# Kernel tuning notes

Measured on AMD Instinct MI355X. Metric: run time of the kernel, lower is better.

Reference implementation:

```python
import jax, jax.numpy as jnp
import numpy as np

B = 8192
D_IN, D1, D2, D3, D_OUT = 784, 256, 1024, 256, 10
N_STEPS = 20
LR_INFER = 0.1
GAMMA = 0.1


def setup_inputs() -> dict:
    key = jax.random.key(0)
    ks = jax.random.split(key, 17)
    inp = {
        "x": jax.random.normal(ks[0], (B, D_IN), dtype=jnp.float32),
        # state inits (original does randn*0.1 inside forward)
        "x1_0": jax.random.normal(ks[1], (B, D1), dtype=jnp.float32) * 0.1,
        "x2_0": jax.random.normal(ks[2], (B, D2), dtype=jnp.float32) * 0.1,
        "x3_0": jax.random.normal(ks[3], (B, D3), dtype=jnp.float32) * 0.1,
        "x4_0": jax.random.normal(ks[4], (B, D_OUT), dtype=jnp.float32) * 0.1,
        # parameters (randn*0.1 per __init__)
        "W1": jax.random.normal(ks[5], (D_IN, D1), dtype=jnp.float32) * 0.1,
        "W2": jax.random.normal(ks[6], (D1, D2), dtype=jnp.float32) * 0.1,
        "W3": jax.random.normal(ks[7], (D2, D3), dtype=jnp.float32) * 0.1,
        "W4": jax.random.normal(ks[8], (D3, D_OUT), dtype=jnp.float32) * 0.1,
        "b1": jnp.zeros((D1,), dtype=jnp.float32),
        "b2": jnp.zeros((D2,), dtype=jnp.float32),
        "b3": jnp.zeros((D3,), dtype=jnp.float32),
        "b4": jnp.zeros((D_OUT,), dtype=jnp.float32),
        "L1": jax.random.normal(ks[9], (D1, D1), dtype=jnp.float32) * 0.1,
        "L2": jax.random.normal(ks[10], (D2, D2), dtype=jnp.float32) * 0.1,
        "L3": jax.random.normal(ks[11], (D3, D3), dtype=jnp.float32) * 0.1,
    }
    return inp


def reference(x, x1_0, x2_0, x3_0, x4_0, W1, W2, W3, W4, b1, b2, b3, b4, L1, L2, L3):
    sig = jax.nn.sigmoid
    # x1_pred depends only on the (constant) input x; compute once.
    x1_pred = sig(x @ W1 + b1)  # [B, D1]

    def step(carry, _):
        x1, x2, x3 = carry
        x3_pred = sig(x2 @ W3 + b3)        # [B, D3]
        x2_pred = sig(x1 @ W2 + b2)        # [B, D2]
        x4_pred = x3 @ W4 + b4             # [B, D_OUT]
        eps4 = x4_pred - x4_0
        eps3 = x3_pred - x3
        eps2 = x2_pred - x2
        eps1 = x1_pred - x1
        x3_grad = -eps3 + eps4 @ W4.T - GAMMA * (x3 @ L3)
        x2_grad = -eps2 + eps3 @ W3.T - GAMMA * (x2 @ L2)
        x1_grad = -eps1 + eps2 @ W2.T - GAMMA * (x1 @ L1)
        return (x1 - LR_INFER * x1_grad,
                x2 - LR_INFER * x2_grad,
                x3 - LR_INFER * x3_grad), None

    (x1, x2, x3), _ = jax.lax.scan(step, (x1_0, x2_0, x3_0), None, length=N_STEPS)
    return x3 @ W4 + b4  # [B, D_OUT]
```

## Files before the change

kernel.cpp:

```cpp
#include <hip/hip_runtime.h>
#include <hip/hip_bf16.h>
#include <cstdint>
#include <cstring>


#define LRC 0.1f

typedef unsigned short u16;
typedef unsigned int u32;
typedef __attribute__((ext_vector_type(4))) float f32x4;
typedef __attribute__((ext_vector_type(8))) __bf16 bf16x8;

__device__ __forceinline__ u16 f2b(float v) {
  __hip_bfloat16 h = __float2bfloat16(v);
  union { __hip_bfloat16 h; u16 u; } c; c.h = h; return c.u;
}
__device__ __forceinline__ float b2f(u16 u) {
  union { u16 u; __hip_bfloat16 h; } c; c.u = u; return __bfloat162float(c.h);
}
__device__ __forceinline__ float sigf(float x) { return 1.0f / (1.0f + expf(-x)); }

__device__ __forceinline__ void gll16(const void* g, void* l) {
  __builtin_amdgcn_global_load_lds((const __attribute__((address_space(1))) u32*)g,
                                   (__attribute__((address_space(3))) u32*)l,
                                   16, 0, 0);
}

struct GemmDesc {
  const u16* A; const u16* Bt;
  const u16* A2; const u16* Bt2;
  const float* bias; const float* master; const float* pred; const float* aux;
  const u16* eprev;
  float* outF; u16* outB;
  int lda, ldb, lda2, ldb2, K, K2, N, tnl, nblocks, epi;
};
struct Descs { GemmDesc d[6]; int nd; };

__global__ __launch_bounds__(256) void k_gemm_multi(Descs P) {
  int bid = blockIdx.x;
  int base = 0, di = 0;
  while (di + 1 < P.nd && bid >= base + P.d[di].nblocks) { base += P.d[di].nblocks; ++di; }
  const GemmDesc& d = P.d[di];
  int t = bid - base;
  int tid = threadIdx.x;

  __shared__ u16 ldsA[8192];
  __shared__ u16 ldsB[8192];

  int w = tid >> 6, l = tid & 63;
  int wm = w & 1, wn = w >> 1;
  int lrow = l & 15, kgrp = l >> 4;

  int tnl = d.tnl;
  int j = t >> 3;
  int tm = (t & 7) * (d.nblocks >> (3 + tnl)) + (j >> tnl);
  int tnn = j & ((1 << tnl) - 1);
  int m0 = tm * 128, n0 = tnn * 128;

  f32x4 zero = {0.f, 0.f, 0.f, 0.f};
  f32x4 acc[4][4];
  #pragma unroll
  for (int a = 0; a < 4; ++a)
    #pragma unroll
    for (int b = 0; b < 4; ++b) acc[a][b] = zero;

  int srow = l >> 2;
  int scol = (l & 3) * 8;

  auto run = [&](const u16* A, int lda, const u16* Bt, int ldb, int K) {
    for (int k0 = 0; k0 < K;) {
      int nsub = (K - k0 >= 64) ? 2 : 1;
      for (int i = 0; i < 2 * nsub; ++i) {
        int c = i * 4 + w;
        int ks = c >> 3, rb = c & 7;
        int row = rb * 16 + srow;
        int col = k0 + ks * 32 + scol;
        gll16(A  + (size_t)(m0 + row) * lda + col, &ldsA[c * 512]);
        gll16(Bt + (size_t)(n0 + row) * ldb + col, &ldsB[c * 512]);
      }
      __syncthreads();
      for (int ks = 0; ks < nsub; ++ks) {
        bf16x8 af[4], bfr[4];
        #pragma unroll
        for (int mi = 0; mi < 4; ++mi)
          af[mi] = *(const bf16x8*)&ldsA[ks * 4096 + (wm * 64 + mi * 16 + lrow) * 32 + kgrp * 8];
        #pragma unroll
        for (int ni = 0; ni < 4; ++ni)
          bfr[ni] = *(const bf16x8*)&ldsB[ks * 4096 + (wn * 64 + ni * 16 + lrow) * 32 + kgrp * 8];
        #pragma unroll
        for (int mi = 0; mi < 4; ++mi)
          #pragma unroll
          for (int ni = 0; ni < 4; ++ni)
            acc[mi][ni] = __builtin_amdgcn_mfma_f32_16x16x32_bf16(af[mi], bfr[ni], acc[mi][ni], 0, 0, 0);
      }
      __syncthreads();
      k0 += nsub * 32;
    }
  };

  run(d.A, d.lda, d.Bt, d.ldb, d.K);
  if (d.K2 > 0) run(d.A2, d.lda2, d.Bt2, d.ldb2, d.K2);

  int epi = d.epi;
  #pragma unroll
  for (int mi = 0; mi < 4; ++mi) {
    #pragma unroll
    for (int ni = 0; ni < 4; ++ni) {
      #pragma unroll
      for (int j2 = 0; j2 < 4; ++j2) {
        int row = m0 + wm * 64 + mi * 16 + kgrp * 4 + j2;
        int col = n0 + wn * 64 + ni * 16 + lrow;
        size_t idx = (size_t)row * d.N + col;
        float a = acc[mi][ni][j2];
        if (epi == 1) {
          float s = sigf(a + d.bias[col]);
          d.outB[idx] = f2b(s - b2f(d.eprev[idx]));
        } else if (epi == 2) {
          d.outF[idx] = sigf(a + d.bias[col]);
        } else if (epi == 3) {
          float v = d.outF[idx];
          float nv = v + LRC * (d.pred[idx] - v) - LRC * a;
          d.outF[idx] = nv; d.outB[idx] = f2b(nv);
        } else if (epi == 4) {
          float v = d.outF[idx];
          float nv = v + LRC * b2f(d.eprev[idx]) - LRC * a;
          d.outF[idx] = nv; d.outB[idx] = f2b(nv);
        } else {
          float v = d.outF[idx];
          float nv = v + LRC * b2f(d.eprev[idx]) - LRC * (a + d.pred[idx]);
          d.outF[idx] = nv; d.outB[idx] = f2b(nv);
        }
      }
    }
  }
}

__global__ void k_state_init(const float* __restrict__ src, float* __restrict__ dstF,
                             u16* __restrict__ dstB, int n) {
  int i = blockIdx.x * 256 + threadIdx.x;
  if (i < n) { float v = src[i]; dstF[i] = v; dstB[i] = f2b(v); }
}
__global__ void k_transpose_scale(const float* __restrict__ src, u16* __restrict__ dst,
                                  int R, int C, float scale) {
  int i = blockIdx.x * 256 + threadIdx.x;
  if (i < R * C) { int r = i / C, c = i - r * C; dst[c * R + r] = f2b(scale * src[i]); }
}
__global__ void k_conv_bf(const float* __restrict__ src, u16* __restrict__ dst, int n) {
  int i = blockIdx.x * 256 + threadIdx.x;
  if (i < n) dst[i] = f2b(src[i]);
}
__global__ void k_m4g(const float* __restrict__ W4, const float* __restrict__ L3,
                      u16* __restrict__ dst) {
  int i = blockIdx.x * 256 + threadIdx.x;
  if (i < 256 * 256) {
    int n = i >> 8, k = i & 255;
    float s = 0.f;
    #pragma unroll
    for (int jj = 0; jj < 10; ++jj) s = fmaf(W4[n * 10 + jj], W4[k * 10 + jj], s);
    dst[i] = f2b(s - 0.1f * L3[k * 256 + n]);
  }
}
__global__ void k_c4(const float* __restrict__ W4, const float* __restrict__ b4,
                     const float* __restrict__ x40, float* __restrict__ dst) {
  int i = blockIdx.x * 256 + threadIdx.x;
  if (i < 8192 * 256) {
    int m = i >> 8, n = i & 255;
    float s = 0.f;
    #pragma unroll
    for (int jj = 0; jj < 10; ++jj) s = fmaf(b4[jj] - x40[m * 10 + jj], W4[n * 10 + jj], s);
    dst[i] = s;
  }
}
__global__ void k_xsplit(const float* __restrict__ x, u16* __restrict__ dst) {
  int i = blockIdx.x * 256 + threadIdx.x;
  if (i < 8192 * 1600) {
    int m = i / 1600, c = i - m * 1600;
    u16 o = 0;
    if (c < 784) o = f2b(x[m * 784 + c]);
    else if (c >= 800 && c < 1584) {
      float v = x[m * 784 + (c - 800)];
      float h = b2f(f2b(v));
      o = f2b(v - h);
    }
    dst[i] = o;
  }
}
__global__ void k_w1c(const float* __restrict__ W1, u16* __restrict__ dst) {
  int i = blockIdx.x * 256 + threadIdx.x;
  if (i < 256 * 1600) {
    int n = i / 1600, c = i - n * 1600;
    u16 o = 0;
    if (c < 784) o = f2b(W1[c * 256 + n]);
    else if (c >= 800 && c < 1584) o = f2b(W1[(c - 800) * 256 + n]);
    dst[i] = o;
  }
}
__global__ void k_final(const float* __restrict__ X3, const float* __restrict__ W4,
                        const float* __restrict__ b4, float* __restrict__ out) {
  int i = blockIdx.x * 256 + threadIdx.x;
  if (i < 8192 * 10) {
    int m = i / 10, n = i - m * 10;
    const float* xr = X3 + (size_t)m * 256;
    float acc = 0.f;
    #pragma unroll 4
    for (int k = 0; k < 256; ++k) acc = fmaf(xr[k], W4[k * 10 + n], acc);
    out[i] = acc + b4[n];
  }
}

extern "C" void kernel_launch(void* const* d_in, const int* in_sizes, int n_in,
                              void* d_out, int out_size, void* d_ws, size_t ws_size,
                              hipStream_t stream) {
  const float* x    = (const float*)d_in[0];
  const float* x1_0 = (const float*)d_in[1];
  const float* x2_0 = (const float*)d_in[2];
  const float* x3_0 = (const float*)d_in[3];
  const float* x4_0 = (const float*)d_in[4];
  const float* W1 = (const float*)d_in[5];
  const float* W2 = (const float*)d_in[6];
  const float* W3 = (const float*)d_in[7];
  const float* W4 = (const float*)d_in[8];
  const float* b1 = (const float*)d_in[9];
  const float* b2 = (const float*)d_in[10];
  const float* b3 = (const float*)d_in[11];
  const float* b4 = (const float*)d_in[12];
  const float* L1 = (const float*)d_in[13];
  const float* L2 = (const float*)d_in[14];
  const float* L3 = (const float*)d_in[15];

  if (ws_size < 143687680u) return;
  char* ws = (char*)d_ws;
  float* X1f   = (float*)(ws + 0);
  float* X2f   = (float*)(ws + 8388608);
  float* X3f   = (float*)(ws + 41943040);
  u16*   X1b[2]= { (u16*)(ws + 50331648), (u16*)(ws + 54525952) };
  u16*   X2b[2]= { (u16*)(ws + 58720256), (u16*)(ws + 75497472) };
  u16*   X3b[2]= { (u16*)(ws + 92274688), (u16*)(ws + 96468992) };
  float* P1    = (float*)(ws + 100663296);
  u16*   E2    = (u16*)(ws + 109051904);
  u16*   E3    = (u16*)(ws + 125829120);
  float* C4    = (float*)(ws + 130023424);
  u16*   XS    = (u16*)(ws + 109051904);
  u16*   W2t   = (u16*)(ws + 138412032);
  u16*   W3t   = (u16*)(ws + 138936320);
  u16*   L1t   = (u16*)(ws + 139460608);
  u16*   L2t   = (u16*)(ws + 139591680);
  u16*   M4G   = (u16*)(ws + 141688832);
  u16*   W2b   = (u16*)(ws + 141819904);
  u16*   W3b   = (u16*)(ws + 142344192);
  u16*   W1c   = (u16*)(ws + 142868480);

  dim3 blk(256);
  auto G = [](int n) { return dim3((unsigned)((n + 255) / 256)); };

  k_state_init<<<G(8192*256),  blk, 0, stream>>>(x1_0, X1f, X1b[0], 8192*256);
  k_state_init<<<G(8192*1024), blk, 0, stream>>>(x2_0, X2f, X2b[0], 8192*1024);
  k_state_init<<<G(8192*256),  blk, 0, stream>>>(x3_0, X3f, X3b[0], 8192*256);
  k_transpose_scale<<<G(256*1024),  blk, 0, stream>>>(W2, W2t, 256, 1024, 1.0f);
  k_transpose_scale<<<G(1024*256),  blk, 0, stream>>>(W3, W3t, 1024, 256, 1.0f);
  k_transpose_scale<<<G(256*256),   blk, 0, stream>>>(L1, L1t, 256, 256, -0.1f);
  k_transpose_scale<<<G(1024*1024), blk, 0, stream>>>(L2, L2t, 1024, 1024, -0.1f);
  k_conv_bf<<<G(256*1024), blk, 0, stream>>>(W2, W2b, 256*1024);
  k_conv_bf<<<G(1024*256), blk, 0, stream>>>(W3, W3b, 1024*256);
  k_m4g<<<G(256*256), blk, 0, stream>>>(W4, L3, M4G);
  k_xsplit<<<G(8192*1600), blk, 0, stream>>>(x, XS);
  k_w1c<<<G(256*1600), blk, 0, stream>>>(W1, W1c);

  auto mkg = [](const u16* A, const u16* Bt, int lda, int ldb, int K, int N,
                int tnl, int nb, int epi) {
    GemmDesc g; memset(&g, 0, sizeof(g));
    g.A = A; g.Bt = Bt; g.lda = lda; g.ldb = ldb; g.K = K; g.N = N;
    g.tnl = tnl; g.nblocks = nb; g.epi = epi;
    return g;
  };

  {
    Descs pp; memset(&pp, 0, sizeof(pp)); pp.nd = 1;
    pp.d[0] = mkg(XS, W1c, 1600, 1600, 1600, 256, 1, 128, 2);
    pp.d[0].bias = b1; pp.d[0].outF = P1;
    k_gemm_multi<<<dim3(128), blk, 0, stream>>>(pp);
  }
  k_c4<<<G(8192*256), blk, 0, stream>>>(W4, b4, x4_0, C4);

  for (int s = 0; s < 20; ++s) {
    int p = s & 1, q = p ^ 1;

    Descs ph1; memset(&ph1, 0, sizeof(ph1)); ph1.nd = 2;
    ph1.d[0] = mkg(X2b[p], W3t, 1024, 1024, 1024, 256, 1, 128, 1);
    ph1.d[0].bias = b3; ph1.d[0].eprev = X3b[p]; ph1.d[0].outB = E3;
    ph1.d[1] = mkg(X1b[p], W2t, 256, 256, 256, 1024, 3, 512, 1);
    ph1.d[1].bias = b2; ph1.d[1].eprev = X2b[p]; ph1.d[1].outB = E2;
    k_gemm_multi<<<dim3(640), blk, 0, stream>>>(ph1);

    Descs ph2; memset(&ph2, 0, sizeof(ph2)); ph2.nd = 3;
    ph2.d[0] = mkg(E3, W3b, 256, 256, 256, 1024, 3, 512, 4);
    ph2.d[0].A2 = X2b[p]; ph2.d[0].Bt2 = L2t; ph2.d[0].lda2 = 1024;
    ph2.d[0].ldb2 = 1024; ph2.d[0].K2 = 1024;
    ph2.d[0].eprev = E2; ph2.d[0].outF = X2f; ph2.d[0].outB = X2b[q];
    ph2.d[1] = mkg(E2, W2b, 1024, 1024, 1024, 256, 1, 128, 3);
    ph2.d[1].A2 = X1b[p]; ph2.d[1].Bt2 = L1t; ph2.d[1].lda2 = 256;
    ph2.d[1].ldb2 = 256; ph2.d[1].K2 = 256;
    ph2.d[1].pred = P1; ph2.d[1].outF = X1f; ph2.d[1].outB = X1b[q];
    ph2.d[2] = mkg(X3b[p], M4G, 256, 256, 256, 256, 1, 128, 6);
    ph2.d[2].eprev = E3; ph2.d[2].pred = C4;
    ph2.d[2].outF = X3f; ph2.d[2].outB = X3b[q];
    k_gemm_multi<<<dim3(768), blk, 0, stream>>>(ph2);
  }

  k_final<<<G(81920), blk, 0, stream>>>(X3f, W4, b4, (float*)d_out);
}
```

Before: 2.333 ms.

## Load A fragments directly to registers with double-buffered prefetch in multi-GEMM kernel

```diff
diff --git a/kernel.cpp b/kernel.cpp
--- a/kernel.cpp
+++ b/kernel.cpp
@@ -44,7 +44,6 @@
   int t = bid - base;
   int tid = threadIdx.x;
 
-  __shared__ u16 ldsA[8192];
   __shared__ u16 ldsB[8192];
 
   int w = tid >> 6, l = tid & 63;
@@ -67,39 +66,66 @@
   int srow = l >> 2;
   int scol = (l & 3) * 8;
 
-  auto run = [&](const u16* A, int lda, const u16* Bt, int ldb, int K) {
-    for (int k0 = 0; k0 < K;) {
-      int nsub = (K - k0 >= 64) ? 2 : 1;
-      for (int i = 0; i < 2 * nsub; ++i) {
-        int c = i * 4 + w;
-        int ks = c >> 3, rb = c & 7;
-        int row = rb * 16 + srow;
-        int col = k0 + ks * 32 + scol;
-        gll16(A  + (size_t)(m0 + row) * lda + col, &ldsA[c * 512]);
-        gll16(Bt + (size_t)(n0 + row) * ldb + col, &ldsB[c * 512]);
-      }
-      __syncthreads();
-      for (int ks = 0; ks < nsub; ++ks) {
-        bf16x8 af[4], bfr[4];
-        #pragma unroll
-        for (int mi = 0; mi < 4; ++mi)
-          af[mi] = *(const bf16x8*)&ldsA[ks * 4096 + (wm * 64 + mi * 16 + lrow) * 32 + kgrp * 8];
+  int T1 = d.K >> 6;
+  int T  = T1 + (d.K2 >> 6);
+
+  auto loadA = [&](int vt, bf16x8* af) {
+    const u16* A; int lda, k0;
+    if (vt < T1) { A = d.A;  lda = d.lda;  k0 = vt << 6; }
+    else         { A = d.A2; lda = d.lda2; k0 = (vt - T1) << 6; }
+    #pragma unroll
+    for (int ks = 0; ks < 2; ++ks)
+      #pragma unroll
+      for (int mi = 0; mi < 4; ++mi)
+        af[ks * 4 + mi] = *(const bf16x8*)(A +
+            (size_t)(m0 + wm * 64 + mi * 16 + lrow) * lda + (k0 + ks * 32 + kgrp * 8));
+  };
+
+  auto stageB = [&](int vt) {
+    const u16* Bt; int ldb, k0;
+    if (vt < T1) { Bt = d.Bt;  ldb = d.ldb;  k0 = vt << 6; }
+    else         { Bt = d.Bt2; ldb = d.ldb2; k0 = (vt - T1) << 6; }
+    #pragma unroll
+    for (int i = 0; i < 4; ++i) {
+      int c = i * 4 + w;
+      int ks = c >> 3, rb = c & 7;
+      gll16(Bt + (size_t)(n0 + rb * 16 + srow) * ldb + (k0 + ks * 32 + scol),
+            &ldsB[c * 512]);
+    }
+  };
+
+  auto compute = [&](const bf16x8* af) {
+    #pragma unroll
+    for (int ks = 0; ks < 2; ++ks) {
+      bf16x8 bfr[4];
+      #pragma unroll
+      for (int ni = 0; ni < 4; ++ni)
+        bfr[ni] = *(const bf16x8*)&ldsB[ks * 4096 + (wn * 64 + ni * 16 + lrow) * 32 + kgrp * 8];
+      #pragma unroll
+      for (int mi = 0; mi < 4; ++mi)
         #pragma unroll
         for (int ni = 0; ni < 4; ++ni)
-          bfr[ni] = *(const bf16x8*)&ldsB[ks * 4096 + (wn * 64 + ni * 16 + lrow) * 32 + kgrp * 8];
-        #pragma unroll
-        for (int mi = 0; mi < 4; ++mi)
-          #pragma unroll
-          for (int ni = 0; ni < 4; ++ni)
-            acc[mi][ni] = __builtin_amdgcn_mfma_f32_16x16x32_bf16(af[mi], bfr[ni], acc[mi][ni], 0, 0, 0);
-      }
-      __syncthreads();
-      k0 += nsub * 32;
+          acc[mi][ni] = __builtin_amdgcn_mfma_f32_16x16x32_bf16(af[ks * 4 + mi], bfr[ni], acc[mi][ni], 0, 0, 0);
     }
   };
 
-  run(d.A, d.lda, d.Bt, d.ldb, d.K);
-  if (d.K2 > 0) run(d.A2, d.lda2, d.Bt2, d.ldb2, d.K2);
+  bf16x8 a0[8], a1[8];
+  loadA(0, a0);
+  stageB(0);
+  __syncthreads();
+  for (int vt = 0; vt < T; vt += 2) {
+    if (vt + 1 < T) loadA(vt + 1, a1);
+    compute(a0);
+    __syncthreads();
+    if (vt + 1 < T) stageB(vt + 1);
+    __syncthreads();
+    if (vt + 1 >= T) break;
+    if (vt + 2 < T) loadA(vt + 2, a0);
+    compute(a1);
+    __syncthreads();
+    if (vt + 2 < T) stageB(vt + 2);
+    __syncthreads();
+  }
 
   int epi = d.epi;
   #pragma unroll
```

Result: slower. 4.954 ms (+112.4%).

## Fuse all iteration GEMM phases into one persistent cooperative kernel with grid sync

Applied to the files above, without the earlier changes.

```diff
diff --git a/kernel.cpp b/kernel.cpp
--- a/kernel.cpp
+++ b/kernel.cpp
@@ -1,10 +1,13 @@
 #include <hip/hip_runtime.h>
 #include <hip/hip_bf16.h>
+#include <hip/hip_cooperative_groups.h>
 #include <cstdint>
 #include <cstring>
 
 
 #define LRC 0.1f
+
+namespace cg = cooperative_groups;
 
 typedef unsigned short u16;
 typedef unsigned int u32;
@@ -35,17 +38,16 @@
   int lda, ldb, lda2, ldb2, K, K2, N, tnl, nblocks, epi;
 };
 struct Descs { GemmDesc d[6]; int nd; };
-
-__global__ __launch_bounds__(256) void k_gemm_multi(Descs P) {
-  int bid = blockIdx.x;
+struct AllDesc { GemmDesc ph1[2][2]; GemmDesc ph2[2][3]; };
+
+__device__ void do_gemm(const GemmDesc* __restrict__ dd, int nd, int bid, int tid) {
   int base = 0, di = 0;
-  while (di + 1 < P.nd && bid >= base + P.d[di].nblocks) { base += P.d[di].nblocks; ++di; }
-  const GemmDesc& d = P.d[di];
+  while (di + 1 < nd && bid >= base + dd[di].nblocks) { base += dd[di].nblocks; ++di; }
+  const GemmDesc& d = dd[di];
   int t = bid - base;
-  int tid = threadIdx.x;
-
-  __shared__ u16 ldsA[8192];
-  __shared__ u16 ldsB[8192];
+
+  static __shared__ u16 ldsA[8192];
+  static __shared__ u16 ldsB[8192];
 
   int w = tid >> 6, l = tid & 63;
   int wm = w & 1, wn = w >> 1;
@@ -135,6 +137,24 @@
   }
 }
 
+__global__ __launch_bounds__(256) void k_gemm_multi(Descs P) {
+  do_gemm(P.d, P.nd, blockIdx.x, threadIdx.x);
+}
+
+__global__ __launch_bounds__(256, 3) void k_steps(AllDesc P) {
+  cg::grid_group g = cg::this_grid();
+  int tid = threadIdx.x;
+  for (int s = 0; s < 20; ++s) {
+    int p = s & 1;
+    for (int job = blockIdx.x; job < 640; job += gridDim.x)
+      do_gemm(P.ph1[p], 2, job, tid);
+    g.sync();
+    for (int job = blockIdx.x; job < 768; job += gridDim.x)
+      do_gemm(P.ph2[p], 3, job, tid);
+    g.sync();
+  }
+}
+
 __global__ void k_state_init(const float* __restrict__ src, float* __restrict__ dstF,
                              u16* __restrict__ dstB, int n) {
   int i = blockIdx.x * 256 + threadIdx.x;
@@ -282,29 +302,40 @@
   }
   k_c4<<<G(8192*256), blk, 0, stream>>>(W4, b4, x4_0, C4);
 
-  for (int s = 0; s < 20; ++s) {
-    int p = s & 1, q = p ^ 1;
-
-    Descs ph1; memset(&ph1, 0, sizeof(ph1)); ph1.nd = 2;
-    ph1.d[0] = mkg(X2b[p], W3t, 1024, 1024, 1024, 256, 1, 128, 1);
-    ph1.d[0].bias = b3; ph1.d[0].eprev = X3b[p]; ph1.d[0].outB = E3;
-    ph1.d[1] = mkg(X1b[p], W2t, 256, 256, 256, 1024, 3, 512, 1);
-    ph1.d[1].bias = b2; ph1.d[1].eprev = X2b[p]; ph1.d[1].outB = E2;
-    k_gemm_multi<<<dim3(640), blk, 0, stream>>>(ph1);
-
-    Descs ph2; memset(&ph2, 0, sizeof(ph2)); ph2.nd = 3;
-    ph2.d[0] = mkg(E3, W3b, 256, 256, 256, 1024, 3, 512, 4);
-    ph2.d[0].A2 = X2b[p]; ph2.d[0].Bt2 = L2t; ph2.d[0].lda2 = 1024;
-    ph2.d[0].ldb2 = 1024; ph2.d[0].K2 = 1024;
-    ph2.d[0].eprev = E2; ph2.d[0].outF = X2f; ph2.d[0].outB = X2b[q];
-    ph2.d[1] = mkg(E2, W2b, 1024, 1024, 1024, 256, 1, 128, 3);
-    ph2.d[1].A2 = X1b[p]; ph2.d[1].Bt2 = L1t; ph2.d[1].lda2 = 256;
-    ph2.d[1].ldb2 = 256; ph2.d[1].K2 = 256;
-    ph2.d[1].pred = P1; ph2.d[1].outF = X1f; ph2.d[1].outB = X1b[q];
-    ph2.d[2] = mkg(X3b[p], M4G, 256, 256, 256, 256, 1, 128, 6);
-    ph2.d[2].eprev = E3; ph2.d[2].pred = C4;
-    ph2.d[2].outF = X3f; ph2.d[2].outB = X3b[q];
-    k_gemm_multi<<<dim3(768), blk, 0, stream>>>(ph2);
+  AllDesc AD; memset(&AD, 0, sizeof(AD));
+  for (int p = 0; p < 2; ++p) {
+    int q = p ^ 1;
+    AD.ph1[p][0] = mkg(X2b[p], W3t, 1024, 1024, 1024, 256, 1, 128, 1);
+    AD.ph1[p][0].bias = b3; AD.ph1[p][0].eprev = X3b[p]; AD.ph1[p][0].outB = E3;
+    AD.ph1[p][1] = mkg(X1b[p], W2t, 256, 256, 256, 1024, 3, 512, 1);
+    AD.ph1[p][1].bias = b2; AD.ph1[p][1].eprev = X2b[p]; AD.ph1[p][1].outB = E2;
+    AD.ph2[p][0] = mkg(E3, W3b, 256, 256, 256, 1024, 3, 512, 4);
+    AD.ph2[p][0].A2 = X2b[p]; AD.ph2[p][0].Bt2 = L2t; AD.ph2[p][0].lda2 = 1024;
+    AD.ph2[p][0].ldb2 = 1024; AD.ph2[p][0].K2 = 1024;
+    AD.ph2[p][0].eprev = E2; AD.ph2[p][0].outF = X2f; AD.ph2[p][0].outB = X2b[q];
+    AD.ph2[p][1] = mkg(E2, W2b, 1024, 1024, 1024, 256, 1, 128, 3);
+    AD.ph2[p][1].A2 = X1b[p]; AD.ph2[p][1].Bt2 = L1t; AD.ph2[p][1].lda2 = 256;
+    AD.ph2[p][1].ldb2 = 256; AD.ph2[p][1].K2 = 256;
+    AD.ph2[p][1].pred = P1; AD.ph2[p][1].outF = X1f; AD.ph2[p][1].outB = X1b[q];
+    AD.ph2[p][2] = mkg(X3b[p], M4G, 256, 256, 256, 256, 1, 128, 6);
+    AD.ph2[p][2].eprev = E3; AD.ph2[p][2].pred = C4;
+    AD.ph2[p][2].outF = X3f; AD.ph2[p][2].outB = X3b[q];
+  }
+
+  void* kargs[] = { (void*)&AD };
+  hipError_t ce = hipLaunchCooperativeKernel((const void*)k_steps, dim3(768), blk,
+                                             kargs, 0, stream);
+  if (ce != hipSuccess) {
+    (void)hipGetLastError();
+    for (int s = 0; s < 20; ++s) {
+      int p = s & 1;
+      Descs d1; memset(&d1, 0, sizeof(d1)); d1.nd = 2;
+      d1.d[0] = AD.ph1[p][0]; d1.d[1] = AD.ph1[p][1];
+      k_gemm_multi<<<dim3(640), blk, 0, stream>>>(d1);
+      Descs d2; memset(&d2, 0, sizeof(d2)); d2.nd = 3;
+      d2.d[0] = AD.ph2[p][0]; d2.d[1] = AD.ph2[p][1]; d2.d[2] = AD.ph2[p][2];
+      k_gemm_multi<<<dim3(768), blk, 0, stream>>>(d2);
+    }
   }
 
   k_final<<<G(81920), blk, 0, stream>>>(X3f, W4, b4, (float*)d_out);
```

Result: slower. 6.204 ms (+165.9%).
